# Performance work log

Hardware: AMD Instinct MI355X
Metric: run time of the kernel (lower is better)

Reference implementation:

```python
import jax, jax.numpy as jnp
import numpy as np

B, N, T, E, H = 2, 512, 12, 128, 8
D = E // H  # head_dim = 16


def setup_inputs() -> dict:
    key = jax.random.key(0)
    ks = jax.random.split(key, 16)
    mk = lambda k, shape, s=1.0: (jax.random.normal(k, shape, dtype=jnp.float32) * s)
    inp = {
        'flow_q': mk(ks[0], (B, N, T, E)),
        'flow_k': mk(ks[1], (B, N, T, E)),
        'flow_v': mk(ks[2], (B, N, T, E)),
        'speed_q': mk(ks[3], (B, N, T, E)),
        'speed_k': mk(ks[4], (B, N, T, E)),
        'speed_v': mk(ks[5], (B, N, T, E)),
        # Linear weights stored as (in, out) so y = x @ W
        'WfQ': mk(ks[6], (E, E), 1.0 / np.sqrt(E)),
        'WfK': mk(ks[7], (E, E), 1.0 / np.sqrt(E)),
        'WfV': mk(ks[8], (E, E), 1.0 / np.sqrt(E)),
        'WsQ': mk(ks[9], (E, E), 1.0 / np.sqrt(E)),
        'WsK': mk(ks[10], (E, E), 1.0 / np.sqrt(E)),
        'WsV': mk(ks[11], (E, E), 1.0 / np.sqrt(E)),
        'Kj': mk(ks[12], (N, 1)),          # FlowSpeed params (xavier ~ small)
        'Vfp': mk(ks[13], (N, 1)),
        'Wout': mk(ks[14], (E, E), 1.0 / np.sqrt(E)),
        'bout': jnp.zeros((E,), dtype=jnp.float32),
    }
    return inp


def _heads(x, W):
    # [B,N,T,C] @ [C,E] -> [B,N,T,H,D] -> [B,H,T,N,D]
    y = jnp.einsum('bntc,ce->bnte', x, W).reshape(B, N, T, H, D)
    return jnp.transpose(y, (0, 3, 2, 1, 4))


def reference(flow_q, flow_k, flow_v, speed_q, speed_k, speed_v,
              WfQ, WfK, WfV, WsQ, WsK, WsV, Kj, Vfp, Wout, bout):
    Qf = _heads(flow_q, WfQ)
    Kf = _heads(flow_k, WfK)
    Vf = _heads(flow_v, WfV)
    Qs = _heads(speed_q, WsQ)
    Ks = _heads(speed_k, WsK)
    Vs = _heads(speed_v, WsV)

    scale = 1.0 / np.sqrt(D)
    # FlowSpeed nonlinearity on Qs; Kj/Vfp (N,1) broadcast over [B,H,T,N,D]
    Qf_from_speed = Kj * (Qs - Qs * Qs / (Vfp + 1e-05))

    att = lambda A, Bm: jax.nn.softmax(
        jnp.einsum('bhtnd,bhtmd->bhtnm', A, Bm) * scale, axis=-1)

    z_ff = att(Qf, Kf)
    z_fs = att(Kf, Qf_from_speed)
    z_sf = att(Ks, Qf)
    z_ss = att(Qs, Ks)

    ctx = lambda z, V: jnp.einsum('bhtnm,bhtmd->bhtnd', z, V)

    def proj_out(c):
        # [B,H,T,N,D] -> [B,N,T,H*D] -> fc_out
        c = jnp.transpose(c, (0, 3, 2, 1, 4)).reshape(B, N, T, E)
        return jnp.einsum('bnte,ef->bntf', c, Wout) + bout

    out_ff = proj_out(ctx(z_ff, Vf))
    out_fs = proj_out(ctx(z_fs, Vf))
    out_sf = proj_out(ctx(z_sf, Vs))
    out_ss = proj_out(ctx(z_ss, Vs))
    return (out_ff, out_fs, out_sf, out_ss)
```

## Files before the change

kernel.cpp:

```cpp
#include <hip/hip_runtime.h>
#include <math.h>

constexpr int Bb = 2, Nn = 512, Tt = 12, Ee = 128, Hh = 8, Dd = 16;
constexpr int NTOK   = Bb * Nn * Tt;
constexpr int PROJ   = NTOK * Ee;
constexpr int SLICES = Bb * Hh * Tt;
constexpr int NSL    = Nn * Dd;
constexpr int SLE    = SLICES * NSL;


struct PtrPack { const float* x[6]; const float* W[6]; };
struct WPack   { const float* W[7]; };

typedef __attribute__((ext_vector_type(8)))  short bf16x8;
typedef __attribute__((ext_vector_type(16))) float f32x16;
union FragU { bf16x8 v; unsigned u[4]; };

__device__ __forceinline__ unsigned pk_bf16(float a, float b) {
  unsigned r;
  asm("v_cvt_pk_bf16_f32 %0, %1, %2" : "=v"(r) : "v"(a), "v"(b));
  return r;
}
__device__ __forceinline__ unsigned short bf16_1(float a) {
  return (unsigned short)(pk_bf16(a, a) & 0xffffu);
}
__device__ __forceinline__ void split_frag(const float e[8], bf16x8& hv, bf16x8& lv) {
  FragU H, L;
  #pragma unroll
  for (int i = 0; i < 4; ++i) {
    const unsigned h = pk_bf16(e[2*i], e[2*i+1]);
    const float h0 = __uint_as_float(h << 16);
    const float h1 = __uint_as_float(h & 0xffff0000u);
    L.u[i] = pk_bf16(e[2*i] - h0, e[2*i+1] - h1);
    H.u[i] = h;
  }
  hv = H.v; lv = L.v;
}

__global__ __launch_bounds__(256) void prep_w_kernel(
    WPack wp, unsigned short* __restrict__ wf)
{
  const int m = blockIdx.x;
  const float* __restrict__ W = wp.W[m];
  for (int e = threadIdx.x; e < 2048; e += 256) {
    const int ct = e >> 9, ks = (e >> 6) & 7, lane = e & 63;
    const int ql = lane & 31, hi = lane >> 5;
    const int c = ct * 32 + ql, k0 = ks * 16 + hi * 8;
    float w[8];
    #pragma unroll
    for (int j = 0; j < 8; ++j) w[j] = W[(size_t)(k0 + j) * Ee + c];
    bf16x8 hv, lv;
    split_frag(w, hv, lv);
    *(bf16x8*)&wf[((size_t)(m * 2 + 0) * 2048 + e) * 8] = hv;
    *(bf16x8*)&wf[((size_t)(m * 2 + 1) * 2048 + e) * 8] = lv;
  }
}

__global__ __launch_bounds__(256) void proj_mfma_kernel(
    PtrPack pp, const float* __restrict__ Kj, const float* __restrict__ Vfp,
    unsigned short* __restrict__ qk, unsigned short* __restrict__ vt,
    const unsigned short* __restrict__ wf)
{
  __shared__ float XS[32][132];
  const int ty = blockIdx.y;
  const int g  = blockIdx.x;
  const int nc = g & 15;
  const int bt = g >> 4;
  const int b  = bt / Tt, t = bt % Tt;
  const int n0 = nc * 32;
  const int wave = threadIdx.x >> 6, lane = threadIdx.x & 63;
  const int ql = lane & 31, hi = lane >> 5;

  f32x16 acc;
  #pragma unroll
  for (int r = 0; r < 16; ++r) acc[r] = 0.f;

  const float* __restrict__ xrow =
      pp.x[ty] + ((size_t)(b * Nn + n0 + ql) * Tt + t) * Ee;
  const unsigned short* __restrict__ wbase =
      wf + ((size_t)(ty * 2) * 2048 + wave * 512 + lane) * 8;

  for (int ks = 0; ks < 8; ++ks) {
    const float4 a0 = *(const float4*)&xrow[ks * 16 + hi * 8];
    const float4 a1 = *(const float4*)&xrow[ks * 16 + hi * 8 + 4];
    float e8[8] = {a0.x, a0.y, a0.z, a0.w, a1.x, a1.y, a1.z, a1.w};
    bf16x8 xh, xl;
    split_frag(e8, xh, xl);
    const bf16x8 wh = *(const bf16x8*)&wbase[(size_t)ks * 512];
    const bf16x8 wl = *(const bf16x8*)&wbase[(size_t)ks * 512 + 2048 * 8];
    acc = __builtin_amdgcn_mfma_f32_32x32x16_bf16(xh, wh, acc, 0, 0, 0);
    acc = __builtin_amdgcn_mfma_f32_32x32x16_bf16(xh, wl, acc, 0, 0, 0);
    acc = __builtin_amdgcn_mfma_f32_32x32x16_bf16(xl, wh, acc, 0, 0, 0);
    if (ty == 3)
      acc = __builtin_amdgcn_mfma_f32_32x32x16_bf16(xl, wl, acc, 0, 0, 0);
  }

  #pragma unroll
  for (int r = 0; r < 16; ++r)
    XS[(r & 3) + 8 * (r >> 2) + 4 * hi][wave * 32 + ql] = acc[r];
  __syncthreads();

  if (ty == 2 || ty == 5) {
    if (threadIdx.x < 128) {
      const int h = threadIdx.x >> 4, d = threadIdx.x & 15;
      const int slice = (b * Hh + h) * Tt + t;
      float v[32];
      #pragma unroll
      for (int n = 0; n < 32; ++n) v[n] = XS[n][h * 16 + d];
      FragU F[4];
      #pragma unroll
      for (int i = 0; i < 16; ++i)
        F[i >> 2].u[i & 3] = pk_bf16(v[2 * i], v[2 * i + 1]);
      unsigned short* __restrict__ dst =
          vt + (size_t)(ty == 5) * SLE + (size_t)slice * NSL + d * 512 + n0;
      #pragma unroll
      for (int i = 0; i < 4; ++i) *(bf16x8*)&dst[i * 8] = F[i].v;
    }
  } else {
    const int h = threadIdx.x >> 5, nn = threadIdx.x & 31;
    const int slice = (b * Hh + h) * Tt + t;
    const int n = n0 + nn;
    float v[16];
    #pragma unroll
    for (int d = 0; d < 16; ++d) v[d] = XS[nn][h * 16 + d];
    FragU HI[2], LO[2];
    #pragma unroll
    for (int i = 0; i < 8; ++i) {
      const unsigned hw = pk_bf16(v[2 * i], v[2 * i + 1]);
      const float h0 = __uint_as_float(hw << 16);
      const float h1 = __uint_as_float(hw & 0xffff0000u);
      HI[i >> 2].u[i & 3] = hw;
      LO[i >> 2].u[i & 3] = pk_bf16(v[2 * i] - h0, v[2 * i + 1] - h1);
    }
    const int s = (ty == 0) ? 0 : (ty == 1) ? 1 : (ty == 3) ? 2 : 3;
    unsigned short* __restrict__ hp =
        qk + (size_t)(s * 2 + 0) * SLE + (size_t)slice * NSL + n * 16;
    unsigned short* __restrict__ lp =
        qk + (size_t)(s * 2 + 1) * SLE + (size_t)slice * NSL + n * 16;
    *(bf16x8*)&hp[0] = HI[0].v;  *(bf16x8*)&hp[8] = HI[1].v;
    *(bf16x8*)&lp[0] = LO[0].v;  *(bf16x8*)&lp[8] = LO[1].v;
    if (ty == 3) {
      const float kj = Kj[n];
      const float iv = 1.0f / (Vfp[n] + 1e-5f);
      float gv[16];
      #pragma unroll
      for (int d = 0; d < 16; ++d) gv[d] = kj * (v[d] - v[d] * v[d] * iv);
      FragU GH[2], GL[2];
      #pragma unroll
      for (int i = 0; i < 8; ++i) {
        const unsigned hw = pk_bf16(gv[2 * i], gv[2 * i + 1]);
        const float h0 = __uint_as_float(hw << 16);
        const float h1 = __uint_as_float(hw & 0xffff0000u);
        GH[i >> 2].u[i & 3] = hw;
        GL[i >> 2].u[i & 3] = pk_bf16(gv[2 * i] - h0, gv[2 * i + 1] - h1);
      }
      unsigned short* __restrict__ gp =
          qk + (size_t)(4 * 2 + 0) * SLE + (size_t)slice * NSL + n * 16;
      unsigned short* __restrict__ glp =
          qk + (size_t)(4 * 2 + 1) * SLE + (size_t)slice * NSL + n * 16;
      *(bf16x8*)&gp[0]  = GH[0].v;  *(bf16x8*)&gp[8]  = GH[1].v;
      *(bf16x8*)&glp[0] = GL[0].v;  *(bf16x8*)&glp[8] = GL[1].v;
    }
  }
}

__global__ __launch_bounds__(512) void attn_mfma_kernel(
    const unsigned short* __restrict__ qk, const unsigned short* __restrict__ vt,
    float* __restrict__ ctx)
{
  const int slice = blockIdx.x;
  const int ty    = blockIdx.y;
  const int a_s[4] = {0, 1, 3, 2};
  const int b_s[4] = {1, 4, 0, 3};
  const int v_s[4] = {0, 0, 1, 1};

  const unsigned short* __restrict__ Ah =
      qk + (size_t)(a_s[ty] * 2 + 0) * SLE + (size_t)slice * NSL;
  const unsigned short* __restrict__ Al =
      qk + (size_t)(a_s[ty] * 2 + 1) * SLE + (size_t)slice * NSL;
  const unsigned short* __restrict__ Kh_ =
      qk + (size_t)(b_s[ty] * 2 + 0) * SLE + (size_t)slice * NSL;
  const unsigned short* __restrict__ Kl_ =
      qk + (size_t)(b_s[ty] * 2 + 1) * SLE + (size_t)slice * NSL;
  const unsigned short* __restrict__ Vt_ =
      vt + (size_t)v_s[ty] * SLE + (size_t)slice * NSL;

  const int tid  = threadIdx.x;
  const int wave = tid >> 6;
  const int lane = tid & 63;
  const int hi   = lane >> 5;
  const int ql   = lane & 31;
  const int q0   = wave * 64;
  const int d15  = ql & 15;

  const float SC = 0.25f * 1.4426950408889634f;

  bf16x8 qh[2], qlo[2];
  #pragma unroll
  for (int qt = 0; qt < 2; ++qt) {
    const int qrow = q0 + qt * 32 + ql;
    qh[qt]  = *(const bf16x8*)&Ah[qrow * 16 + hi * 8];
    qlo[qt] = *(const bf16x8*)&Al[qrow * 16 + hi * 8];
  }

  f32x16 Z;
  #pragma unroll
  for (int r = 0; r < 16; ++r) Z[r] = 0.0f;

  f32x16 o[2];
  float  l_[2] = {0.0f, 0.0f};
  float  m_[2];
  m_[0] = m_[1] = (ty == 1) ? -1e30f : 0.0f;
  #pragma unroll
  for (int qt = 0; qt < 2; ++qt)
    #pragma unroll
    for (int r = 0; r < 16; ++r) o[qt][r] = 0.0f;

  for (int kc = 0; kc < Nn; kc += 32) {
    const int krow = kc + ql;
    const bf16x8 kh = *(const bf16x8*)&Kh_[krow * 16 + hi * 8];
    const bf16x8 kl = *(const bf16x8*)&Kl_[krow * 16 + hi * 8];
    const bf16x8 vb0 = *(const bf16x8*)&Vt_[d15 * 512 + kc + hi * 8];
    const bf16x8 vb1 = *(const bf16x8*)&Vt_[d15 * 512 + kc + 16 + hi * 8];

    #pragma unroll
    for (int qt = 0; qt < 2; ++qt) {
      f32x16 S;
      S = __builtin_amdgcn_mfma_f32_32x32x16_bf16(kh, qh[qt],  Z, 0, 0, 0);
      S = __builtin_amdgcn_mfma_f32_32x32x16_bf16(kh, qlo[qt], S, 0, 0, 0);
      S = __builtin_amdgcn_mfma_f32_32x32x16_bf16(kl, qh[qt],  S, 0, 0, 0);
      if (ty == 1)
        S = __builtin_amdgcn_mfma_f32_32x32x16_bf16(kl, qlo[qt], S, 0, 0, 0);

      if (ty == 1) {
        float smax = S[0];
        #pragma unroll
        for (int r = 1; r < 16; ++r) smax = fmaxf(smax, S[r]);
        float cm = smax * SC;
        cm = fmaxf(cm, __shfl_xor(cm, 32));
        if (!__all(cm <= m_[qt] + 8.0f)) {
          const float nm = fmaxf(m_[qt], cm);
          const float f  = exp2f(m_[qt] - nm);
          l_[qt] *= f;
          #pragma unroll
          for (int r = 0; r < 16; ++r) {
            const int qloc = (r & 3) + 8 * (r >> 2) + 4 * hi;
            o[qt][r] *= __shfl(f, qloc);
          }
          m_[qt] = nm;
        }
      }

      float p[16];
      float ls = 0.0f;
      #pragma unroll
      for (int r = 0; r < 16; ++r) {
        p[r] = exp2f(fmaf(S[r], SC, -m_[qt]));
        ls += p[r];
      }
      l_[qt] += ls;

      FragU pa0, pa1;
      {
        const unsigned wa = pk_bf16(p[0],  p[1]);
        const unsigned wb = pk_bf16(p[2],  p[3]);
        const unsigned wc = pk_bf16(p[4],  p[5]);
        const unsigned wd = pk_bf16(p[6],  p[7]);
        const unsigned swa = __shfl_xor(wa, 32);
        const unsigned swb = __shfl_xor(wb, 32);
        const unsigned swc = __shfl_xor(wc, 32);
        const unsigned swd = __shfl_xor(wd, 32);
        pa0.u[0] = hi ? swc : wa;
        pa0.u[1] = hi ? swd : wb;
        pa0.u[2] = hi ? wc  : swa;
        pa0.u[3] = hi ? wd  : swb;
        const unsigned we = pk_bf16(p[8],  p[9]);
        const unsigned wf_ = pk_bf16(p[10], p[11]);
        const unsigned wg = pk_bf16(p[12], p[13]);
        const unsigned wh = pk_bf16(p[14], p[15]);
        const unsigned swe = __shfl_xor(we, 32);
        const unsigned swf = __shfl_xor(wf_, 32);
        const unsigned swg = __shfl_xor(wg, 32);
        const unsigned swh = __shfl_xor(wh, 32);
        pa1.u[0] = hi ? swg : we;
        pa1.u[1] = hi ? swh : wf_;
        pa1.u[2] = hi ? wg  : swe;
        pa1.u[3] = hi ? wh  : swf;
      }
      o[qt] = __builtin_amdgcn_mfma_f32_32x32x16_bf16(pa0.v, vb0, o[qt], 0, 0, 0);
      o[qt] = __builtin_amdgcn_mfma_f32_32x32x16_bf16(pa1.v, vb1, o[qt], 0, 0, 0);
    }
  }

  const int b = slice / (Hh * Tt);
  const int h = (slice / Tt) % Hh;
  const int t = slice % Tt;
  float* __restrict__ outp = ctx + (size_t)ty * PROJ;
  #pragma unroll
  for (int qt = 0; qt < 2; ++qt) {
    const float lsum = l_[qt] + __shfl_xor(l_[qt], 32);
    const float linv = 1.0f / lsum;
    #pragma unroll
    for (int r = 0; r < 16; ++r) {
      const int qloc = (r & 3) + 8 * (r >> 2) + 4 * hi;
      const float lr = __shfl(linv, qloc);
      if (ql < 16) {
        const int n = q0 + qt * 32 + qloc;
        outp[(((size_t)b * Nn + n) * Tt + t) * Ee + h * Dd + ql] = o[qt][r] * lr;
      }
    }
  }
}

__global__ __launch_bounds__(256) void out_mfma_kernel(
    const float* __restrict__ ctx, const unsigned short* __restrict__ wf,
    const float* __restrict__ bout, float* __restrict__ out)
{
  const int ty   = blockIdx.y;
  const int tok0 = blockIdx.x * 32;
  const int wave = threadIdx.x >> 6;
  const int lane = threadIdx.x & 63;
  const int ql = lane & 31, hi = lane >> 5;

  f32x16 acc;
  #pragma unroll
  for (int r = 0; r < 16; ++r) acc[r] = 0.f;

  const float* __restrict__ xrow =
      ctx + (size_t)ty * PROJ + (size_t)(tok0 + ql) * Ee;
  const unsigned short* __restrict__ wbase =
      wf + ((size_t)(6 * 2) * 2048 + wave * 512 + lane) * 8;

  for (int ks = 0; ks < 8; ++ks) {
    const float4 a0 = *(const float4*)&xrow[ks * 16 + hi * 8];
    const float4 a1 = *(const float4*)&xrow[ks * 16 + hi * 8 + 4];
    float e8[8] = {a0.x, a0.y, a0.z, a0.w, a1.x, a1.y, a1.z, a1.w};
    bf16x8 xh, xl;
    split_frag(e8, xh, xl);
    const bf16x8 wh = *(const bf16x8*)&wbase[(size_t)ks * 512];
    const bf16x8 wl = *(const bf16x8*)&wbase[(size_t)ks * 512 + 2048 * 8];
    acc = __builtin_amdgcn_mfma_f32_32x32x16_bf16(xh, wh, acc, 0, 0, 0);
    acc = __builtin_amdgcn_mfma_f32_32x32x16_bf16(xh, wl, acc, 0, 0, 0);
    acc = __builtin_amdgcn_mfma_f32_32x32x16_bf16(xl, wh, acc, 0, 0, 0);
  }

  const int c = wave * 32 + ql;
  const float bc = bout[c];
  #pragma unroll
  for (int r = 0; r < 16; ++r) {
    const int tok = tok0 + (r & 3) + 8 * (r >> 2) + 4 * hi;
    out[(size_t)ty * PROJ + (size_t)tok * Ee + c] = acc[r] + bc;
  }
}

extern "C" void kernel_launch(void* const* d_in, const int* in_sizes, int n_in,
                              void* d_out, int out_size, void* d_ws, size_t ws_size,
                              hipStream_t stream) {
  const float* fq  = (const float*)d_in[0];
  const float* fk  = (const float*)d_in[1];
  const float* fv  = (const float*)d_in[2];
  const float* sq  = (const float*)d_in[3];
  const float* sk  = (const float*)d_in[4];
  const float* sv  = (const float*)d_in[5];
  const float* WfQ = (const float*)d_in[6];
  const float* WfK = (const float*)d_in[7];
  const float* WfV = (const float*)d_in[8];
  const float* WsQ = (const float*)d_in[9];
  const float* WsK = (const float*)d_in[10];
  const float* WsV = (const float*)d_in[11];
  const float* Kj  = (const float*)d_in[12];
  const float* Vfp = (const float*)d_in[13];
  const float* Wout = (const float*)d_in[14];
  const float* bout = (const float*)d_in[15];

  unsigned short* qk = (unsigned short*)d_ws;
  unsigned short* vt = qk + (size_t)10 * SLE;
  unsigned short* wf = vt + (size_t)2 * SLE;
  float* ctx = (float*)(wf + 229376);

  PtrPack pp;
  pp.x[0] = fq; pp.x[1] = fk; pp.x[2] = fv;
  pp.x[3] = sq; pp.x[4] = sk; pp.x[5] = sv;
  pp.W[0] = WfQ; pp.W[1] = WfK; pp.W[2] = WfV;
  pp.W[3] = WsQ; pp.W[4] = WsK; pp.W[5] = WsV;
  WPack wp;
  wp.W[0] = WfQ; wp.W[1] = WfK; wp.W[2] = WfV;
  wp.W[3] = WsQ; wp.W[4] = WsK; wp.W[5] = WsV; wp.W[6] = Wout;

  prep_w_kernel<<<7, 256, 0, stream>>>(wp, wf);
  proj_mfma_kernel<<<dim3(384, 6), 256, 0, stream>>>(pp, Kj, Vfp, qk, vt, wf);
  attn_mfma_kernel<<<dim3(SLICES, 4), 512, 0, stream>>>(qk, vt, ctx);
  out_mfma_kernel<<<dim3(NTOK / 32, 4), 256, 0, stream>>>(ctx, wf, bout, (float*)d_out);
}
```

Measured before the change: 229.0 us.

## Fold softmax scale into weights, ones-column row sums, LDS-staged GEMM I/O

```diff
diff --git a/kernel.cpp b/kernel.cpp
--- a/kernel.cpp
+++ b/kernel.cpp
@@ -6,7 +6,9 @@
 constexpr int PROJ   = NTOK * Ee;
 constexpr int SLICES = Bb * Hh * Tt;
 constexpr int NSL    = Nn * Dd;
-constexpr int SLE    = SLICES * NSL;
+constexpr long SLE   = (long)SLICES * NSL;
+constexpr int NSL17  = 17 * 512;
+constexpr long SLE17 = (long)SLICES * NSL17;
 
 
 struct PtrPack { const float* x[6]; const float* W[6]; };
@@ -20,9 +22,6 @@
   unsigned r;
   asm("v_cvt_pk_bf16_f32 %0, %1, %2" : "=v"(r) : "v"(a), "v"(b));
   return r;
-}
-__device__ __forceinline__ unsigned short bf16_1(float a) {
-  return (unsigned short)(pk_bf16(a, a) & 0xffffu);
 }
 __device__ __forceinline__ void split_frag(const float e[8], bf16x8& hv, bf16x8& lv) {
   FragU H, L;
@@ -41,6 +40,8 @@
     WPack wp, unsigned short* __restrict__ wf)
 {
   const int m = blockIdx.x;
+  const float SQ = sqrtf(0.25f * 1.4426950408889634f);
+  const float scale = (m == 0 || m == 1 || m == 3 || m == 4) ? SQ : 1.0f;
   const float* __restrict__ W = wp.W[m];
   for (int e = threadIdx.x; e < 2048; e += 256) {
     const int ct = e >> 9, ks = (e >> 6) & 7, lane = e & 63;
@@ -48,7 +49,7 @@
     const int c = ct * 32 + ql, k0 = ks * 16 + hi * 8;
     float w[8];
     #pragma unroll
-    for (int j = 0; j < 8; ++j) w[j] = W[(size_t)(k0 + j) * Ee + c];
+    for (int j = 0; j < 8; ++j) w[j] = W[(size_t)(k0 + j) * Ee + c] * scale;
     bf16x8 hv, lv;
     split_frag(w, hv, lv);
     *(bf16x8*)&wf[((size_t)(m * 2 + 0) * 2048 + e) * 8] = hv;
@@ -68,22 +69,29 @@
   const int bt = g >> 4;
   const int b  = bt / Tt, t = bt % Tt;
   const int n0 = nc * 32;
-  const int wave = threadIdx.x >> 6, lane = threadIdx.x & 63;
+  const int tid = threadIdx.x;
+  const int wave = tid >> 6, lane = tid & 63;
   const int ql = lane & 31, hi = lane >> 5;
 
+  const float* __restrict__ xg = pp.x[ty];
+  for (int i = tid; i < 1024; i += 256) {
+    const int row = i >> 5, ch = i & 31;
+    *(float4*)&XS[row][ch * 4] =
+        *(const float4*)&xg[((size_t)(b * Nn + n0 + row) * Tt + t) * Ee + ch * 4];
+  }
+  __syncthreads();
+
   f32x16 acc;
   #pragma unroll
   for (int r = 0; r < 16; ++r) acc[r] = 0.f;
 
-  const float* __restrict__ xrow =
-      pp.x[ty] + ((size_t)(b * Nn + n0 + ql) * Tt + t) * Ee;
   const unsigned short* __restrict__ wbase =
       wf + ((size_t)(ty * 2) * 2048 + wave * 512 + lane) * 8;
 
   for (int ks = 0; ks < 8; ++ks) {
-    const float4 a0 = *(const float4*)&xrow[ks * 16 + hi * 8];
-    const float4 a1 = *(const float4*)&xrow[ks * 16 + hi * 8 + 4];
-    float e8[8] = {a0.x, a0.y, a0.z, a0.w, a1.x, a1.y, a1.z, a1.w};
+    float e8[8];
+    *(float4*)&e8[0] = *(const float4*)&XS[ql][ks * 16 + hi * 8];
+    *(float4*)&e8[4] = *(const float4*)&XS[ql][ks * 16 + hi * 8 + 4];
     bf16x8 xh, xl;
     split_frag(e8, xh, xl);
     const bf16x8 wh = *(const bf16x8*)&wbase[(size_t)ks * 512];
@@ -94,6 +102,7 @@
     if (ty == 3)
       acc = __builtin_amdgcn_mfma_f32_32x32x16_bf16(xl, wl, acc, 0, 0, 0);
   }
+  __syncthreads();
 
   #pragma unroll
   for (int r = 0; r < 16; ++r)
@@ -101,9 +110,10 @@
   __syncthreads();
 
   if (ty == 2 || ty == 5) {
-    if (threadIdx.x < 128) {
-      const int h = threadIdx.x >> 4, d = threadIdx.x & 15;
+    if (tid < 128) {
+      const int h = tid >> 4, d = tid & 15;
       const int slice = (b * Hh + h) * Tt + t;
+      const long vsel = (ty == 5);
       float v[32];
       #pragma unroll
       for (int n = 0; n < 32; ++n) v[n] = XS[n][h * 16 + d];
@@ -112,12 +122,21 @@
       for (int i = 0; i < 16; ++i)
         F[i >> 2].u[i & 3] = pk_bf16(v[2 * i], v[2 * i + 1]);
       unsigned short* __restrict__ dst =
-          vt + (size_t)(ty == 5) * SLE + (size_t)slice * NSL + d * 512 + n0;
+          vt + vsel * SLE17 + (size_t)slice * NSL17 + d * 512 + n0;
       #pragma unroll
       for (int i = 0; i < 4; ++i) *(bf16x8*)&dst[i * 8] = F[i].v;
+      if (d == 0) {
+        FragU O_;
+        #pragma unroll
+        for (int i = 0; i < 4; ++i) O_.u[i] = 0x3F803F80u;
+        unsigned short* __restrict__ op =
+            vt + vsel * SLE17 + (size_t)slice * NSL17 + 16 * 512 + n0;
+        #pragma unroll
+        for (int i = 0; i < 4; ++i) *(bf16x8*)&op[i * 8] = O_.v;
+      }
     }
   } else {
-    const int h = threadIdx.x >> 5, nn = threadIdx.x & 31;
+    const int h = tid >> 5, nn = tid & 31;
     const int slice = (b * Hh + h) * Tt + t;
     const int n = n0 + nn;
     float v[16];
@@ -140,11 +159,16 @@
     *(bf16x8*)&hp[0] = HI[0].v;  *(bf16x8*)&hp[8] = HI[1].v;
     *(bf16x8*)&lp[0] = LO[0].v;  *(bf16x8*)&lp[8] = LO[1].v;
     if (ty == 3) {
+      const float SQ  = sqrtf(0.25f * 1.4426950408889634f);
+      const float RSQ = 1.0f / SQ;
       const float kj = Kj[n];
       const float iv = 1.0f / (Vfp[n] + 1e-5f);
       float gv[16];
       #pragma unroll
-      for (int d = 0; d < 16; ++d) gv[d] = kj * (v[d] - v[d] * v[d] * iv);
+      for (int d = 0; d < 16; ++d) {
+        const float vq = v[d] * RSQ;
+        gv[d] = SQ * (kj * (vq - vq * vq * iv));
+      }
       FragU GH[2], GL[2];
       #pragma unroll
       for (int i = 0; i < 8; ++i) {
@@ -183,7 +207,7 @@
   const unsigned short* __restrict__ Kl_ =
       qk + (size_t)(b_s[ty] * 2 + 1) * SLE + (size_t)slice * NSL;
   const unsigned short* __restrict__ Vt_ =
-      vt + (size_t)v_s[ty] * SLE + (size_t)slice * NSL;
+      vt + (size_t)v_s[ty] * SLE17 + (size_t)slice * NSL17;
 
   const int tid  = threadIdx.x;
   const int wave = tid >> 6;
@@ -191,9 +215,8 @@
   const int hi   = lane >> 5;
   const int ql   = lane & 31;
   const int q0   = wave * 64;
-  const int d15  = ql & 15;
-
-  const float SC = 0.25f * 1.4426950408889634f;
+  const int dv   = (ql < 16) ? ql : 16;
+  const unsigned short* __restrict__ vbase = Vt_ + dv * 512;
 
   bf16x8 qh[2], qlo[2];
   #pragma unroll
@@ -208,9 +231,7 @@
   for (int r = 0; r < 16; ++r) Z[r] = 0.0f;
 
   f32x16 o[2];
-  float  l_[2] = {0.0f, 0.0f};
-  float  m_[2];
-  m_[0] = m_[1] = (ty == 1) ? -1e30f : 0.0f;
+  float  m_[2] = {-1e30f, -1e30f};
   #pragma unroll
   for (int qt = 0; qt < 2; ++qt)
     #pragma unroll
@@ -220,8 +241,8 @@
     const int krow = kc + ql;
     const bf16x8 kh = *(const bf16x8*)&Kh_[krow * 16 + hi * 8];
     const bf16x8 kl = *(const bf16x8*)&Kl_[krow * 16 + hi * 8];
-    const bf16x8 vb0 = *(const bf16x8*)&Vt_[d15 * 512 + kc + hi * 8];
-    const bf16x8 vb1 = *(const bf16x8*)&Vt_[d15 * 512 + kc + 16 + hi * 8];
+    const bf16x8 vb0 = *(const bf16x8*)&vbase[kc + hi * 8];
+    const bf16x8 vb1 = *(const bf16x8*)&vbase[kc + 16 + hi * 8];
 
     #pragma unroll
     for (int qt = 0; qt < 2; ++qt) {
@@ -232,16 +253,15 @@
       if (ty == 1)
         S = __builtin_amdgcn_mfma_f32_32x32x16_bf16(kl, qlo[qt], S, 0, 0, 0);
 
+      float p[16];
       if (ty == 1) {
         float smax = S[0];
         #pragma unroll
         for (int r = 1; r < 16; ++r) smax = fmaxf(smax, S[r]);
-        float cm = smax * SC;
-        cm = fmaxf(cm, __shfl_xor(cm, 32));
+        float cm = fmaxf(smax, __shfl_xor(smax, 32));
         if (!__all(cm <= m_[qt] + 8.0f)) {
           const float nm = fmaxf(m_[qt], cm);
-          const float f  = exp2f(m_[qt] - nm);
-          l_[qt] *= f;
+          const float f  = __builtin_amdgcn_exp2f(m_[qt] - nm);
           #pragma unroll
           for (int r = 0; r < 16; ++r) {
             const int qloc = (r & 3) + 8 * (r >> 2) + 4 * hi;
@@ -249,16 +269,14 @@
           }
           m_[qt] = nm;
         }
-      }
-
-      float p[16];
-      float ls = 0.0f;
-      #pragma unroll
-      for (int r = 0; r < 16; ++r) {
-        p[r] = exp2f(fmaf(S[r], SC, -m_[qt]));
-        ls += p[r];
-      }
-      l_[qt] += ls;
+        #pragma unroll
+        for (int r = 0; r < 16; ++r)
+          p[r] = __builtin_amdgcn_exp2f(S[r] - m_[qt]);
+      } else {
+        #pragma unroll
+        for (int r = 0; r < 16; ++r)
+          p[r] = __builtin_amdgcn_exp2f(S[r]);
+      }
 
       FragU pa0, pa1;
       {
@@ -296,17 +314,17 @@
   const int h = (slice / Tt) % Hh;
   const int t = slice % Tt;
   float* __restrict__ outp = ctx + (size_t)ty * PROJ;
+  const int lsrc = (lane & 32) | 16;
   #pragma unroll
   for (int qt = 0; qt < 2; ++qt) {
-    const float lsum = l_[qt] + __shfl_xor(l_[qt], 32);
-    const float linv = 1.0f / lsum;
     #pragma unroll
     for (int r = 0; r < 16; ++r) {
       const int qloc = (r & 3) + 8 * (r >> 2) + 4 * hi;
-      const float lr = __shfl(linv, qloc);
+      const float lsum = __shfl(o[qt][r], lsrc);
       if (ql < 16) {
         const int n = q0 + qt * 32 + qloc;
-        outp[(((size_t)b * Nn + n) * Tt + t) * Ee + h * Dd + ql] = o[qt][r] * lr;
+        outp[(((size_t)b * Nn + n) * Tt + t) * Ee + h * Dd + ql] =
+            o[qt][r] * __builtin_amdgcn_rcpf(lsum);
       }
     }
   }
@@ -316,25 +334,29 @@
     const float* __restrict__ ctx, const unsigned short* __restrict__ wf,
     const float* __restrict__ bout, float* __restrict__ out)
 {
+  __shared__ float XS[32][132];
   const int ty   = blockIdx.y;
   const int tok0 = blockIdx.x * 32;
-  const int wave = threadIdx.x >> 6;
-  const int lane = threadIdx.x & 63;
+  const int tid  = threadIdx.x;
+  const int wave = tid >> 6, lane = tid & 63;
   const int ql = lane & 31, hi = lane >> 5;
 
+  const float* __restrict__ src = ctx + (size_t)ty * PROJ + (size_t)tok0 * Ee;
+  for (int i = tid; i < 1024; i += 256)
+    *(float4*)&XS[i >> 5][(i & 31) * 4] = *(const float4*)&src[i * 4];
+  __syncthreads();
+
   f32x16 acc;
   #pragma unroll
   for (int r = 0; r < 16; ++r) acc[r] = 0.f;
 
-  const float* __restrict__ xrow =
-      ctx + (size_t)ty * PROJ + (size_t)(tok0 + ql) * Ee;
   const unsigned short* __restrict__ wbase =
       wf + ((size_t)(6 * 2) * 2048 + wave * 512 + lane) * 8;
 
   for (int ks = 0; ks < 8; ++ks) {
-    const float4 a0 = *(const float4*)&xrow[ks * 16 + hi * 8];
-    const float4 a1 = *(const float4*)&xrow[ks * 16 + hi * 8 + 4];
-    float e8[8] = {a0.x, a0.y, a0.z, a0.w, a1.x, a1.y, a1.z, a1.w};
+    float e8[8];
+    *(float4*)&e8[0] = *(const float4*)&XS[ql][ks * 16 + hi * 8];
+    *(float4*)&e8[4] = *(const float4*)&XS[ql][ks * 16 + hi * 8 + 4];
     bf16x8 xh, xl;
     split_frag(e8, xh, xl);
     const bf16x8 wh = *(const bf16x8*)&wbase[(size_t)ks * 512];
@@ -343,13 +365,20 @@
     acc = __builtin_amdgcn_mfma_f32_32x32x16_bf16(xh, wl, acc, 0, 0, 0);
     acc = __builtin_amdgcn_mfma_f32_32x32x16_bf16(xl, wh, acc, 0, 0, 0);
   }
-
-  const int c = wave * 32 + ql;
-  const float bc = bout[c];
-  #pragma unroll
-  for (int r = 0; r < 16; ++r) {
-    const int tok = tok0 + (r & 3) + 8 * (r >> 2) + 4 * hi;
-    out[(size_t)ty * PROJ + (size_t)tok * Ee + c] = acc[r] + bc;
+  __syncthreads();
+
+  #pragma unroll
+  for (int r = 0; r < 16; ++r)
+    XS[(r & 3) + 8 * (r >> 2) + 4 * hi][wave * 32 + ql] = acc[r];
+  __syncthreads();
+
+  float* __restrict__ dst = out + (size_t)ty * PROJ + (size_t)tok0 * Ee;
+  for (int i = tid; i < 1024; i += 256) {
+    const int row = i >> 5, c4 = (i & 31) * 4;
+    float4 v = *(float4*)&XS[row][c4];
+    const float4 bv = *(const float4*)&bout[c4];
+    v.x += bv.x; v.y += bv.y; v.z += bv.z; v.w += bv.w;
+    *(float4*)&dst[i * 4] = v;
   }
 }
 
@@ -375,7 +404,7 @@
 
   unsigned short* qk = (unsigned short*)d_ws;
   unsigned short* vt = qk + (size_t)10 * SLE;
-  unsigned short* wf = vt + (size_t)2 * SLE;
+  unsigned short* wf = vt + (size_t)2 * SLE17;
   float* ctx = (float*)(wf + 229376);
 
   PtrPack pp;
```

Measured after the change: 195.1 us. 14.8% less time.
